# Optimization experiments

Measured on AMD Instinct MI355X. Metric: run time of the kernel, lower is better.

Reference implementation:

```python
import jax, jax.numpy as jnp
import numpy as np

T, B, H, L = 512, 64, 512, 2  # seq_len, batch, hidden(=input_size), num_layers


def setup_inputs() -> dict:
    key = jax.random.key(0)
    ks = jax.random.split(key, 5)
    std = 1.0 / np.sqrt(H)
    u = lambda k, s: jax.random.uniform(k, s, jnp.float32, -std, std)
    Wxh = u(ks[0], (L, 4 * H, H))   # [L, 4H, in] (in == H here)
    Whh = u(ks[1], (L, 4 * H, H))   # [L, 4H, H]
    bxh = u(ks[2], (L, 4 * H))
    bhh = u(ks[3], (L, 4 * H))
    # LSTMCell.reset_parameters sets the forget-gate bias slice [H:2H] to 1/H
    bxh = bxh.at[:, H:2 * H].set(1.0 / H)
    bhh = bhh.at[:, H:2 * H].set(1.0 / H)
    x = jax.random.normal(ks[4], (T, B, H), jnp.float32)  # [seq, batch, input]
    return {"x": x, "Wxh": Wxh, "Whh": Whh, "bxh": bxh, "bhh": bhh}


def _lstm_forward(x, Wxh, Whh, bxh, bhh):
    n_layers = Wxh.shape[0]
    bsz = x.shape[1]
    hid = Whh.shape[2]
    h0 = jnp.zeros((n_layers, bsz, hid), x.dtype)  # zero init (hc=None path)
    c0 = jnp.zeros((n_layers, bsz, hid), x.dtype)

    def step(carry, x_t):
        h, c = carry  # each [L, B, H]
        h_new, c_new = [], []
        inp = x_t  # [B, in]
        for l in range(n_layers):
            # gate order matches chunk(4): input, forget, cell, output
            gates = inp @ Wxh[l].T + bxh[l] + h[l] @ Whh[l].T + bhh[l]  # [B, 4H]
            i, f, g, o = jnp.split(gates, 4, axis=-1)
            c_l = jax.nn.sigmoid(f) * c[l] + jax.nn.sigmoid(i) * jnp.tanh(g)
            h_l = jax.nn.sigmoid(o) * jnp.tanh(c_l)
            h_new.append(h_l)
            c_new.append(c_l)
            inp = h_l  # feed to next layer
        return (jnp.stack(h_new), jnp.stack(c_new)), h_new[-1]

    (hT, cT), out = jax.lax.scan(step, (h0, c0), x)
    # out: [T, B, H] (top-layer hidden per step); hidden state tuple (h, c): [L, B, H]
    return out, (hT, cT)


def reference(x, Wxh, Whh, bxh, bhh):
    return _lstm_forward(x, Wxh, Whh, bxh, bhh)
```

## Files before the change

### kernel.cpp

```cpp
#include <hip/hip_runtime.h>


#define T_SEQ 512

typedef short s16x8 __attribute__((ext_vector_type(8)));
typedef int   i32x4 __attribute__((ext_vector_type(4)));
typedef float f32x4 __attribute__((ext_vector_type(4)));

__device__ __forceinline__ short f2bf(float f) {
    unsigned u = __builtin_bit_cast(unsigned, f);
    unsigned r = (u + 0x7fffu + ((u >> 16) & 1u)) >> 16;
    return (short)r;
}
__device__ __forceinline__ float sigf(float x) { return 1.0f / (1.0f + __expf(-x)); }
__device__ __forceinline__ float tanhff(float x) { return 2.0f * sigf(2.0f * x) - 1.0f; }

__global__ __launch_bounds__(256) void xcast_kernel(const float* __restrict__ x,
                                                    short* __restrict__ xb) {
    int i = (blockIdx.x * 256 + threadIdx.x) * 8;
    float4 a = *(const float4*)(x + i);
    float4 b = *(const float4*)(x + i + 4);
    s16x8 v;
    v[0]=f2bf(a.x); v[1]=f2bf(a.y); v[2]=f2bf(a.z); v[3]=f2bf(a.w);
    v[4]=f2bf(b.x); v[5]=f2bf(b.y); v[6]=f2bf(b.z); v[7]=f2bf(b.w);
    *(s16x8*)(xb + i) = v;
}

__global__ __launch_bounds__(256) void wpack_kernel(const float* __restrict__ Wxh,
                                                    const float* __restrict__ Whh,
                                                    short* __restrict__ wp) {
    int fg = blockIdx.x * 256 + threadIdx.x;
    int lane = fg & 63;
    int kk   = (fg >> 6)  & 7;
    int g    = (fg >> 9)  & 3;
    int w    = (fg >> 11) & 3;
    int bb   = (fg >> 13) & 31;
    int l    = (fg >> 18) & 1;
    int ksrc = w * 128 + (kk & 3) * 32 + (lane >> 4) * 8;
    int jp   = g * 512 + bb * 16 + (lane & 15);
    const float* src = (kk < 4) ? (Wxh + ((size_t)(l * 2048 + jp) * 512 + ksrc))
                                : (Whh + ((size_t)(l * 2048 + jp) * 512 + ksrc));
    float4 a = *(const float4*)src;
    float4 b = *(const float4*)(src + 4);
    s16x8 v;
    v[0]=f2bf(a.x); v[1]=f2bf(a.y); v[2]=f2bf(a.z); v[3]=f2bf(a.w);
    v[4]=f2bf(b.x); v[5]=f2bf(b.y); v[6]=f2bf(b.z); v[7]=f2bf(b.w);
    *(s16x8*)(wp + (size_t)fg * 8) = v;
}

__device__ __forceinline__ void load4_c(i32x4 af[4], const short* base) {
    asm volatile(
        "global_load_dwordx4 %0, %4, off sc0 sc1\n\t"
        "global_load_dwordx4 %1, %4, off offset:64 sc0 sc1\n\t"
        "global_load_dwordx4 %2, %4, off offset:128 sc0 sc1\n\t"
        "global_load_dwordx4 %3, %4, off offset:192 sc0 sc1\n\t"
        "s_waitcnt vmcnt(0)"
        : "=&v"(af[0]), "=&v"(af[1]), "=&v"(af[2]), "=&v"(af[3])
        : "v"(base)
        : "memory");
}

__device__ __forceinline__ void load8_c(i32x4 ar[4], i32x4 ai[4],
                                        const short* b0, const short* b1) {
    asm volatile(
        "global_load_dwordx4 %0, %8, off sc0 sc1\n\t"
        "global_load_dwordx4 %1, %8, off offset:64 sc0 sc1\n\t"
        "global_load_dwordx4 %2, %8, off offset:128 sc0 sc1\n\t"
        "global_load_dwordx4 %3, %8, off offset:192 sc0 sc1\n\t"
        "global_load_dwordx4 %4, %9, off sc0 sc1\n\t"
        "global_load_dwordx4 %5, %9, off offset:64 sc0 sc1\n\t"
        "global_load_dwordx4 %6, %9, off offset:128 sc0 sc1\n\t"
        "global_load_dwordx4 %7, %9, off offset:192 sc0 sc1\n\t"
        "s_waitcnt vmcnt(0)"
        : "=&v"(ar[0]), "=&v"(ar[1]), "=&v"(ar[2]), "=&v"(ar[3]),
          "=&v"(ai[0]), "=&v"(ai[1]), "=&v"(ai[2]), "=&v"(ai[3])
        : "v"(b0), "v"(b1)
        : "memory");
}

__device__ __forceinline__ void waitf2(const unsigned* fa, int ta,
                                       const unsigned* fb, int tb, int lane) {
    if (ta <= 0 && tb <= 0) return;
    const unsigned* pa = fa + (lane & 31);
    const unsigned* pb = fb + (lane & 31);
    int v0, v1;
    do {
        asm volatile("global_load_dword %0, %2, off sc0 sc1\n\t"
                     "global_load_dword %1, %3, off sc0 sc1\n\t"
                     "s_waitcnt vmcnt(0)"
                     : "=&v"(v0), "=&v"(v1)
                     : "v"(pa), "v"(pb) : "memory");
    } while (v0 < ta || v1 < tb);
}

__global__ __launch_bounds__(256, 1) void lstm_persist(
    const short* __restrict__ xb,
    const short* __restrict__ wp,
    short* __restrict__ h0r,
    short* __restrict__ h1r,
    const float* __restrict__ bxh,
    const float* __restrict__ bhh,
    float* __restrict__ out,
    unsigned* flags) {

    const int l    = blockIdx.x >> 7;
    const int g    = (blockIdx.x >> 5) & 3;
    const int bb   = blockIdx.x & 31;
    const int tid  = threadIdx.x;
    const int wv   = tid >> 6;
    const int lane = tid & 63;

    __shared__ float red[16 * 288];

    s16x8 breg[4][8];
    {
        const short* wb = wp + (size_t)((l * 32 + bb) * 4 + wv) * 16384 + lane * 8;
        #pragma unroll
        for (int g4 = 0; g4 < 4; ++g4)
            #pragma unroll
            for (int kk = 0; kk < 8; ++kk)
                breg[g4][kk] = *(const s16x8*)(wb + (g4 * 8 + kk) * 512);
    }

    const int em = tid >> 4;
    const int ec = tid & 15;
    const int ej = bb * 16 + ec;
    float bsum[4];
    #pragma unroll
    for (int g4 = 0; g4 < 4; ++g4)
        bsum[g4] = bxh[l * 2048 + g4 * 512 + ej] + bhh[l * 2048 + g4 * 512 + ej];

    float creg = 0.f;

    const int arow  = lane & 15;
    const int acol  = wv * 128 + (lane >> 4) * 8;
    const int aboff = (g * 16 + arow) * 512 + acol;

    const unsigned* fown = flags + (l * 4 + g) * 32;
    const unsigned* foth = flags + ((1 - l) * 4 + g) * 32;
    unsigned* myflag = flags + (l * 4 + g) * 32 + bb;

    for (int t = 0; t < T_SEQ; ++t) {
        f32x4 acc[4];
        #pragma unroll
        for (int g4 = 0; g4 < 4; ++g4)
            acc[g4] = (f32x4){0.f, 0.f, 0.f, 0.f};

        if (l == 0) {
            const short* ab = xb + (size_t)t * 32768 + aboff;
            s16x8 ax[4];
            #pragma unroll
            for (int kk = 0; kk < 4; ++kk)
                ax[kk] = *(const s16x8*)(ab + kk * 32);
            #pragma unroll
            for (int kk = 0; kk < 4; ++kk)
                #pragma unroll
                for (int g4 = 0; g4 < 4; ++g4)
                    acc[g4] = __builtin_amdgcn_mfma_f32_16x16x32_bf16(
                        ax[kk], breg[g4][kk], acc[g4], 0, 0, 0);
            waitf2(fown, t, foth, t - 7, lane);
            i32x4 af[4];
            load4_c(af, h0r + (size_t)(t & 7) * 32768 + aboff);
            #pragma unroll
            for (int kk = 0; kk < 4; ++kk)
                #pragma unroll
                for (int g4 = 0; g4 < 4; ++g4)
                    acc[g4] = __builtin_amdgcn_mfma_f32_16x16x32_bf16(
                        __builtin_bit_cast(s16x8, af[kk]),
                        breg[g4][4 + kk], acc[g4], 0, 0, 0);
        } else {
            waitf2(fown, t, foth, t + 1, lane);
            i32x4 af[4], ag[4];
            load8_c(af, ag, h1r + (size_t)(t & 7) * 32768 + aboff,
                            h0r + (size_t)((t + 1) & 7) * 32768 + aboff);
            #pragma unroll
            for (int kk = 0; kk < 4; ++kk)
                #pragma unroll
                for (int g4 = 0; g4 < 4; ++g4)
                    acc[g4] = __builtin_amdgcn_mfma_f32_16x16x32_bf16(
                        __builtin_bit_cast(s16x8, af[kk]),
                        breg[g4][4 + kk], acc[g4], 0, 0, 0);
            #pragma unroll
            for (int kk = 0; kk < 4; ++kk)
                #pragma unroll
                for (int g4 = 0; g4 < 4; ++g4)
                    acc[g4] = __builtin_amdgcn_mfma_f32_16x16x32_bf16(
                        __builtin_bit_cast(s16x8, ag[kk]),
                        breg[g4][kk], acc[g4], 0, 0, 0);
        }

        #pragma unroll
        for (int g4 = 0; g4 < 4; ++g4)
            #pragma unroll
            for (int q = 0; q < 4; ++q)
                red[(wv * 4 + g4) * 288
                    + ((lane >> 4) * 4 + q) * 18 + (lane & 15)] = acc[g4][q];
        __syncthreads();

        float cg[4];
        #pragma unroll
        for (int g4 = 0; g4 < 4; ++g4) {
            float s = bsum[g4];
            #pragma unroll
            for (int w = 0; w < 4; ++w)
                s += red[(w * 4 + g4) * 288 + em * 18 + ec];
            cg[g4] = s;
        }

        float cn = sigf(cg[1]) * creg + sigf(cg[0]) * tanhff(cg[2]);
        float hv = sigf(cg[3]) * tanhff(cn);
        creg = cn;

        {
            short* hring = (l == 0) ? h0r : h1r;
            short* hp = hring + (size_t)((t + 1) & 7) * 32768
                      + (g * 16 + em) * 512 + ej;
            int hb = (int)(unsigned short)f2bf(hv);
            asm volatile("global_store_short %0, %1, off sc0 sc1"
                         :: "v"(hp), "v"(hb) : "memory");
        }
        if (l == 1)
            out[(size_t)t * 32768 + (size_t)(g * 16 + em) * 512 + ej] = hv;
        if (t == T_SEQ - 1) {
            size_t base = (size_t)T_SEQ * 32768;
            out[base + (size_t)(l * 64 + g * 16 + em) * 512 + ej] = hv;
            out[base + 65536 + (size_t)(l * 64 + g * 16 + em) * 512 + ej] = creg;
        }

        asm volatile("s_waitcnt vmcnt(0)" ::: "memory");
        __syncthreads();
        if (tid == 0) {
            int fv = t + 1;
            asm volatile("global_store_dword %0, %1, off sc0 sc1"
                         :: "v"(myflag), "v"(fv) : "memory");
        }
    }
}

extern "C" void kernel_launch(void* const* d_in, const int* in_sizes, int n_in,
                              void* d_out, int out_size, void* d_ws, size_t ws_size,
                              hipStream_t stream) {
    const float* x   = (const float*)d_in[0];
    const float* Wxh = (const float*)d_in[1];
    const float* Whh = (const float*)d_in[2];
    const float* bxh = (const float*)d_in[3];
    const float* bhh = (const float*)d_in[4];
    float* out = (float*)d_out;

    char* ws = (char*)d_ws;
    short*    xb    = (short*)(ws);
    short*    wpk   = (short*)(ws + 33554432);
    short*    h0r   = (short*)(ws + 41943040);
    short*    h1r   = (short*)(ws + 42467328);
    unsigned* flags = (unsigned*)(ws + 42991616);

    hipMemsetAsync(ws + 41943040, 0, 1049600, stream);

    xcast_kernel<<<dim3(8192), dim3(256), 0, stream>>>(x, xb);
    wpack_kernel<<<dim3(2048), dim3(256), 0, stream>>>(Wxh, Whh, wpk);

    lstm_persist<<<dim3(256), dim3(256), 0, stream>>>(xb, wpk, h0r, h1r,
                                                      bxh, bhh, out, flags);
}
```

Before: 1.877 ms.

## Prefetch sync flags speculatively and split layer loops to overlap polling with loads

Splits the persistent LSTM loop into separate layer-0 and layer-1 paths. Each path issues its flag reads early, before the x-projection MFMAs in layer 0 and after the previous step's flag store in layer 1, so the common case needs no blocking poll. In layer 1 the layer-0 hidden-state load is issued as soon as its own flag is satisfied, overlapping it with the wait on the layer-1 dependency. Empty asm barriers pin the weight and bias registers. The aim is to shorten the per-step cross-block synchronization latency on the serial critical path, at the cost of more intricate vmcnt ordering that must stay correct.

```diff
diff --git a/kernel.cpp b/kernel.cpp
--- a/kernel.cpp
+++ b/kernel.cpp
@@ -48,7 +48,7 @@
     *(s16x8*)(wp + (size_t)fg * 8) = v;
 }
 
-__device__ __forceinline__ void load4_c(i32x4 af[4], const short* base) {
+__device__ __forceinline__ void load4_l3(i32x4 af[4], const short* base) {
     asm volatile(
         "global_load_dwordx4 %0, %4, off sc0 sc1\n\t"
         "global_load_dwordx4 %1, %4, off offset:64 sc0 sc1\n\t"
@@ -56,42 +56,92 @@
         "global_load_dwordx4 %3, %4, off offset:192 sc0 sc1\n\t"
         "s_waitcnt vmcnt(0)"
         : "=&v"(af[0]), "=&v"(af[1]), "=&v"(af[2]), "=&v"(af[3])
-        : "v"(base)
-        : "memory");
-}
-
-__device__ __forceinline__ void load8_c(i32x4 ar[4], i32x4 ai[4],
-                                        const short* b0, const short* b1) {
+        : "v"(base) : "memory");
+}
+__device__ __forceinline__ void load4_l3_issue(i32x4 af[4], const short* base) {
     asm volatile(
-        "global_load_dwordx4 %0, %8, off sc0 sc1\n\t"
-        "global_load_dwordx4 %1, %8, off offset:64 sc0 sc1\n\t"
-        "global_load_dwordx4 %2, %8, off offset:128 sc0 sc1\n\t"
-        "global_load_dwordx4 %3, %8, off offset:192 sc0 sc1\n\t"
-        "global_load_dwordx4 %4, %9, off sc0 sc1\n\t"
-        "global_load_dwordx4 %5, %9, off offset:64 sc0 sc1\n\t"
-        "global_load_dwordx4 %6, %9, off offset:128 sc0 sc1\n\t"
-        "global_load_dwordx4 %7, %9, off offset:192 sc0 sc1\n\t"
-        "s_waitcnt vmcnt(0)"
-        : "=&v"(ar[0]), "=&v"(ar[1]), "=&v"(ar[2]), "=&v"(ar[3]),
-          "=&v"(ai[0]), "=&v"(ai[1]), "=&v"(ai[2]), "=&v"(ai[3])
-        : "v"(b0), "v"(b1)
-        : "memory");
-}
-
-__device__ __forceinline__ void waitf2(const unsigned* fa, int ta,
-                                       const unsigned* fb, int tb, int lane) {
-    if (ta <= 0 && tb <= 0) return;
+        "global_load_dwordx4 %0, %4, off sc0 sc1\n\t"
+        "global_load_dwordx4 %1, %4, off offset:64 sc0 sc1\n\t"
+        "global_load_dwordx4 %2, %4, off offset:128 sc0 sc1\n\t"
+        "global_load_dwordx4 %3, %4, off offset:192 sc0 sc1"
+        : "=&v"(af[0]), "=&v"(af[1]), "=&v"(af[2]), "=&v"(af[3])
+        : "v"(base) : "memory");
+}
+__device__ __forceinline__ void tie4(i32x4 af[4]) {
+    asm volatile("s_waitcnt vmcnt(0)"
+                 : "+v"(af[0]), "+v"(af[1]), "+v"(af[2]), "+v"(af[3]) :: "memory");
+}
+
+__device__ __forceinline__ void flag_issue(int* v0, int* v1,
+                                           const unsigned* fa, const unsigned* fb,
+                                           int lane) {
     const unsigned* pa = fa + (lane & 31);
     const unsigned* pb = fb + (lane & 31);
-    int v0, v1;
+    asm volatile("global_load_dword %0, %2, off sc0 sc1\n\t"
+                 "global_load_dword %1, %3, off sc0 sc1"
+                 : "=&v"(*v0), "=&v"(*v1) : "v"(pa), "v"(pb) : "memory");
+}
+__device__ __forceinline__ void tie2_0(int* a, int* b) {
+    asm volatile("s_waitcnt vmcnt(0)" : "+v"(*a), "+v"(*b) :: "memory");
+}
+__device__ __forceinline__ void tie2_1(int* a, int* b) {
+    asm volatile("s_waitcnt vmcnt(1)" : "+v"(*a), "+v"(*b) :: "memory");
+}
+
+__device__ __forceinline__ void pollf(const unsigned* f, int thr, int lane) {
+    if (thr <= 0) return;
+    const unsigned* p = f + (lane & 31);
+    int v;
     do {
-        asm volatile("global_load_dword %0, %2, off sc0 sc1\n\t"
-                     "global_load_dword %1, %3, off sc0 sc1\n\t"
+        asm volatile("global_load_dword %0, %1, off sc0 sc1\n\t"
                      "s_waitcnt vmcnt(0)"
-                     : "=&v"(v0), "=&v"(v1)
-                     : "v"(pa), "v"(pb) : "memory");
-    } while (v0 < ta || v1 < tb);
-}
+                     : "=&v"(v) : "v"(p) : "memory");
+    } while (v < thr);
+}
+__device__ __forceinline__ void pollf2(const unsigned* fa, int ta,
+                                       const unsigned* fb, int tb, int lane) {
+    const unsigned* p = (lane < 32) ? (fa + lane) : (fb + (lane - 32));
+    int thr = (lane < 32) ? ta : tb;
+    int v;
+    do {
+        asm volatile("global_load_dword %0, %1, off sc0 sc1\n\t"
+                     "s_waitcnt vmcnt(0)"
+                     : "=&v"(v) : "v"(p) : "memory");
+    } while (v < thr);
+}
+
+__device__ __forceinline__ void sth_l3(short* p, int bits) {
+    asm volatile("global_store_short %0, %1, off sc0 sc1" :: "v"(p), "v"(bits) : "memory");
+}
+__device__ __forceinline__ void stf_l3(unsigned* p, int v) {
+    asm volatile("global_store_dword %0, %1, off sc0 sc1" :: "v"(p), "v"(v) : "memory");
+}
+
+#define DRAIN() asm volatile("s_waitcnt vmcnt(0)" ::: "memory")
+
+#define MFMA16(FR, WS)                                                        \
+    _Pragma("unroll") for (int kk = 0; kk < 4; ++kk)                          \
+    _Pragma("unroll") for (int g4 = 0; g4 < 4; ++g4)                          \
+        acc[g4] = __builtin_amdgcn_mfma_f32_16x16x32_bf16(                    \
+            __builtin_bit_cast(s16x8, FR[kk]), breg[g4][(WS) + kk],           \
+            acc[g4], 0, 0, 0);
+
+#define REDUCE_EPILOGUE()                                                     \
+    _Pragma("unroll") for (int g4 = 0; g4 < 4; ++g4)                          \
+        _Pragma("unroll") for (int q = 0; q < 4; ++q)                         \
+            red[(wv * 4 + g4) * 288                                           \
+                + ((lane >> 4) * 4 + q) * 18 + (lane & 15)] = acc[g4][q];     \
+    __syncthreads();                                                          \
+    float cg[4];                                                              \
+    _Pragma("unroll") for (int g4 = 0; g4 < 4; ++g4) {                        \
+        float s = bsum[g4];                                                   \
+        _Pragma("unroll") for (int w = 0; w < 4; ++w)                         \
+            s += red[(w * 4 + g4) * 288 + em * 18 + ec];                      \
+        cg[g4] = s;                                                           \
+    }                                                                         \
+    float cn = sigf(cg[1]) * creg + sigf(cg[0]) * tanhff(cg[2]);              \
+    hv = sigf(cg[3]) * tanhff(cn);                                            \
+    creg = cn;
 
 __global__ __launch_bounds__(256, 1) void lstm_persist(
     const short* __restrict__ xb,
@@ -121,6 +171,11 @@
             for (int kk = 0; kk < 8; ++kk)
                 breg[g4][kk] = *(const s16x8*)(wb + (g4 * 8 + kk) * 512);
     }
+    #pragma unroll
+    for (int g4 = 0; g4 < 4; ++g4)
+        asm volatile("" : "+v"(breg[g4][0]), "+v"(breg[g4][1]), "+v"(breg[g4][2]),
+                          "+v"(breg[g4][3]), "+v"(breg[g4][4]), "+v"(breg[g4][5]),
+                          "+v"(breg[g4][6]), "+v"(breg[g4][7]));
 
     const int em = tid >> 4;
     const int ec = tid & 15;
@@ -129,8 +184,9 @@
     #pragma unroll
     for (int g4 = 0; g4 < 4; ++g4)
         bsum[g4] = bxh[l * 2048 + g4 * 512 + ej] + bhh[l * 2048 + g4 * 512 + ej];
-
-    float creg = 0.f;
+    asm volatile("" : "+v"(bsum[0]), "+v"(bsum[1]), "+v"(bsum[2]), "+v"(bsum[3]));
+
+    float creg = 0.f, hv = 0.f;
 
     const int arow  = lane & 15;
     const int acol  = wv * 128 + (lane >> 4) * 8;
@@ -138,103 +194,72 @@
 
     const unsigned* fown = flags + (l * 4 + g) * 32;
     const unsigned* foth = flags + ((1 - l) * 4 + g) * 32;
-    unsigned* myflag = flags + (l * 4 + g) * 32 + bb;
-
-    for (int t = 0; t < T_SEQ; ++t) {
-        f32x4 acc[4];
-        #pragma unroll
-        for (int g4 = 0; g4 < 4; ++g4)
-            acc[g4] = (f32x4){0.f, 0.f, 0.f, 0.f};
-
-        if (l == 0) {
+    unsigned* myflag = (unsigned*)fown + bb;
+
+    if (l == 0) {
+        for (int t = 0; t < T_SEQ; ++t) {
+            int pv0 = 0, pv1 = 0;
+            flag_issue(&pv0, &pv1, fown, foth, lane);
+
+            f32x4 acc[4];
+            #pragma unroll
+            for (int g4 = 0; g4 < 4; ++g4) acc[g4] = (f32x4){0.f,0.f,0.f,0.f};
+
             const short* ab = xb + (size_t)t * 32768 + aboff;
             s16x8 ax[4];
             #pragma unroll
             for (int kk = 0; kk < 4; ++kk)
                 ax[kk] = *(const s16x8*)(ab + kk * 32);
-            #pragma unroll
-            for (int kk = 0; kk < 4; ++kk)
-                #pragma unroll
-                for (int g4 = 0; g4 < 4; ++g4)
-                    acc[g4] = __builtin_amdgcn_mfma_f32_16x16x32_bf16(
-                        ax[kk], breg[g4][kk], acc[g4], 0, 0, 0);
-            waitf2(fown, t, foth, t - 7, lane);
+            MFMA16(ax, 0)
+
+            tie2_0(&pv0, &pv1);
+            if (pv0 < t || pv1 < t - 7) pollf2(fown, t, foth, t - 7, lane);
+
             i32x4 af[4];
-            load4_c(af, h0r + (size_t)(t & 7) * 32768 + aboff);
-            #pragma unroll
-            for (int kk = 0; kk < 4; ++kk)
-                #pragma unroll
-                for (int g4 = 0; g4 < 4; ++g4)
-                    acc[g4] = __builtin_amdgcn_mfma_f32_16x16x32_bf16(
-                        __builtin_bit_cast(s16x8, af[kk]),
-                        breg[g4][4 + kk], acc[g4], 0, 0, 0);
-        } else {
-            waitf2(fown, t, foth, t + 1, lane);
-            i32x4 af[4], ag[4];
-            load8_c(af, ag, h1r + (size_t)(t & 7) * 32768 + aboff,
-                            h0r + (size_t)((t + 1) & 7) * 32768 + aboff);
-            #pragma unroll
-            for (int kk = 0; kk < 4; ++kk)
-                #pragma unroll
-                for (int g4 = 0; g4 < 4; ++g4)
-                    acc[g4] = __builtin_amdgcn_mfma_f32_16x16x32_bf16(
-                        __builtin_bit_cast(s16x8, af[kk]),
-                        breg[g4][4 + kk], acc[g4], 0, 0, 0);
-            #pragma unroll
-            for (int kk = 0; kk < 4; ++kk)
-                #pragma unroll
-                for (int g4 = 0; g4 < 4; ++g4)
-                    acc[g4] = __builtin_amdgcn_mfma_f32_16x16x32_bf16(
-                        __builtin_bit_cast(s16x8, ag[kk]),
-                        breg[g4][kk], acc[g4], 0, 0, 0);
+            load4_l3(af, h0r + (size_t)(t & 7) * 32768 + aboff);
+            MFMA16(af, 4)
+
+            REDUCE_EPILOGUE()
+
+            sth_l3(h0r + (size_t)((t + 1) & 7) * 32768 + (g * 16 + em) * 512 + ej,
+                   (int)(unsigned short)f2bf(hv));
+            DRAIN();
+            __syncthreads();
+            if (tid == 0) stf_l3(myflag, t + 1);
         }
-
-        #pragma unroll
-        for (int g4 = 0; g4 < 4; ++g4)
-            #pragma unroll
-            for (int q = 0; q < 4; ++q)
-                red[(wv * 4 + g4) * 288
-                    + ((lane >> 4) * 4 + q) * 18 + (lane & 15)] = acc[g4][q];
-        __syncthreads();
-
-        float cg[4];
-        #pragma unroll
-        for (int g4 = 0; g4 < 4; ++g4) {
-            float s = bsum[g4];
-            #pragma unroll
-            for (int w = 0; w < 4; ++w)
-                s += red[(w * 4 + g4) * 288 + em * 18 + ec];
-            cg[g4] = s;
-        }
-
-        float cn = sigf(cg[1]) * creg + sigf(cg[0]) * tanhff(cg[2]);
-        float hv = sigf(cg[3]) * tanhff(cn);
-        creg = cn;
-
-        {
-            short* hring = (l == 0) ? h0r : h1r;
-            short* hp = hring + (size_t)((t + 1) & 7) * 32768
-                      + (g * 16 + em) * 512 + ej;
-            int hb = (int)(unsigned short)f2bf(hv);
-            asm volatile("global_store_short %0, %1, off sc0 sc1"
-                         :: "v"(hp), "v"(hb) : "memory");
-        }
-        if (l == 1)
+    } else {
+        int pw0 = 0, pw1 = 0;
+        for (int t = 0; t < T_SEQ; ++t) {
+            tie2_1(&pw0, &pw1);
+            if (pw1 < t + 1) pollf(foth, t + 1, lane);
+            i32x4 ag[4];
+            load4_l3_issue(ag, h0r + (size_t)((t + 1) & 7) * 32768 + aboff);
+            if (pw0 < t) pollf(fown, t, lane);
+            i32x4 af[4];
+            load4_l3(af, h1r + (size_t)(t & 7) * 32768 + aboff);
+            tie4(ag);
+
+            f32x4 acc[4];
+            #pragma unroll
+            for (int g4 = 0; g4 < 4; ++g4) acc[g4] = (f32x4){0.f,0.f,0.f,0.f};
+            MFMA16(af, 4)
+            MFMA16(ag, 0)
+
+            REDUCE_EPILOGUE()
+
+            sth_l3(h1r + (size_t)((t + 1) & 7) * 32768 + (g * 16 + em) * 512 + ej,
+                   (int)(unsigned short)f2bf(hv));
+            DRAIN();
+            __syncthreads();
+            if (tid == 0) stf_l3(myflag, t + 1);
+            flag_issue(&pw0, &pw1, fown, foth, lane);
             out[(size_t)t * 32768 + (size_t)(g * 16 + em) * 512 + ej] = hv;
-        if (t == T_SEQ - 1) {
-            size_t base = (size_t)T_SEQ * 32768;
-            out[base + (size_t)(l * 64 + g * 16 + em) * 512 + ej] = hv;
-            out[base + 65536 + (size_t)(l * 64 + g * 16 + em) * 512 + ej] = creg;
-        }
-
-        asm volatile("s_waitcnt vmcnt(0)" ::: "memory");
-        __syncthreads();
-        if (tid == 0) {
-            int fv = t + 1;
-            asm volatile("global_store_dword %0, %1, off sc0 sc1"
-                         :: "v"(myflag), "v"(fv) : "memory");
         }
     }
+
+    size_t base = (size_t)T_SEQ * 32768;
+    out[base + (size_t)(l * 64 + g * 16 + em) * 512 + ej] = hv;
+    out[base + 65536 + (size_t)(l * 64 + g * 16 + em) * 512 + ej] = creg;
 }
 
 extern "C" void kernel_launch(void* const* d_in, const int* in_sizes, int n_in,
```

Result: slower. 2.793 ms (+48.9%).

## Split K across eight waves per block in persistent LSTM kernel

Applied to the files above, without the earlier changes.

Doubles the threads per block from 256 to 512 so each of eight waves covers 64 of the K dimension instead of 128. This halves the per-wave weight registers, the per-step global loads and the MFMA chain length. The weight packing layout and the shared-memory reduction change to match, and only the first 256 threads do the gate nonlinearity and the stores. The cost is a larger LDS reduction over eight partials and more waves taking part in each per-step barrier.

```diff
diff --git a/kernel.cpp b/kernel.cpp
--- a/kernel.cpp
+++ b/kernel.cpp
@@ -31,14 +31,14 @@
                                                     short* __restrict__ wp) {
     int fg = blockIdx.x * 256 + threadIdx.x;
     int lane = fg & 63;
-    int kk   = (fg >> 6)  & 7;
-    int g    = (fg >> 9)  & 3;
-    int w    = (fg >> 11) & 3;
+    int kk   = (fg >> 6)  & 3;
+    int g    = (fg >> 8)  & 3;
+    int w    = (fg >> 10) & 7;
     int bb   = (fg >> 13) & 31;
     int l    = (fg >> 18) & 1;
-    int ksrc = w * 128 + (kk & 3) * 32 + (lane >> 4) * 8;
+    int ksrc = w * 64 + (kk & 1) * 32 + (lane >> 4) * 8;
     int jp   = g * 512 + bb * 16 + (lane & 15);
-    const float* src = (kk < 4) ? (Wxh + ((size_t)(l * 2048 + jp) * 512 + ksrc))
+    const float* src = (kk < 2) ? (Wxh + ((size_t)(l * 2048 + jp) * 512 + ksrc))
                                 : (Whh + ((size_t)(l * 2048 + jp) * 512 + ksrc));
     float4 a = *(const float4*)src;
     float4 b = *(const float4*)(src + 4);
@@ -48,32 +48,23 @@
     *(s16x8*)(wp + (size_t)fg * 8) = v;
 }
 
-__device__ __forceinline__ void load4_c(i32x4 af[4], const short* base) {
+__device__ __forceinline__ void load2_l3(i32x4 af[2], const short* base) {
+    asm volatile(
+        "global_load_dwordx4 %0, %2, off sc0 sc1\n\t"
+        "global_load_dwordx4 %1, %2, off offset:64 sc0 sc1\n\t"
+        "s_waitcnt vmcnt(0)"
+        : "=&v"(af[0]), "=&v"(af[1])
+        : "v"(base) : "memory");
+}
+__device__ __forceinline__ void load4_c(i32x4 ar[2], i32x4 ai[2],
+                                        const short* b0, const short* b1) {
     asm volatile(
         "global_load_dwordx4 %0, %4, off sc0 sc1\n\t"
         "global_load_dwordx4 %1, %4, off offset:64 sc0 sc1\n\t"
-        "global_load_dwordx4 %2, %4, off offset:128 sc0 sc1\n\t"
-        "global_load_dwordx4 %3, %4, off offset:192 sc0 sc1\n\t"
+        "global_load_dwordx4 %2, %5, off sc0 sc1\n\t"
+        "global_load_dwordx4 %3, %5, off offset:64 sc0 sc1\n\t"
         "s_waitcnt vmcnt(0)"
-        : "=&v"(af[0]), "=&v"(af[1]), "=&v"(af[2]), "=&v"(af[3])
-        : "v"(base)
-        : "memory");
-}
-
-__device__ __forceinline__ void load8_c(i32x4 ar[4], i32x4 ai[4],
-                                        const short* b0, const short* b1) {
-    asm volatile(
-        "global_load_dwordx4 %0, %8, off sc0 sc1\n\t"
-        "global_load_dwordx4 %1, %8, off offset:64 sc0 sc1\n\t"
-        "global_load_dwordx4 %2, %8, off offset:128 sc0 sc1\n\t"
-        "global_load_dwordx4 %3, %8, off offset:192 sc0 sc1\n\t"
-        "global_load_dwordx4 %4, %9, off sc0 sc1\n\t"
-        "global_load_dwordx4 %5, %9, off offset:64 sc0 sc1\n\t"
-        "global_load_dwordx4 %6, %9, off offset:128 sc0 sc1\n\t"
-        "global_load_dwordx4 %7, %9, off offset:192 sc0 sc1\n\t"
-        "s_waitcnt vmcnt(0)"
-        : "=&v"(ar[0]), "=&v"(ar[1]), "=&v"(ar[2]), "=&v"(ar[3]),
-          "=&v"(ai[0]), "=&v"(ai[1]), "=&v"(ai[2]), "=&v"(ai[3])
+        : "=&v"(ar[0]), "=&v"(ar[1]), "=&v"(ai[0]), "=&v"(ai[1])
         : "v"(b0), "v"(b1)
         : "memory");
 }
@@ -93,7 +84,23 @@
     } while (v0 < ta || v1 < tb);
 }
 
-__global__ __launch_bounds__(256, 1) void lstm_persist(
+__device__ __forceinline__ void sth_l3(short* p, int bits) {
+    asm volatile("global_store_short %0, %1, off sc0 sc1" :: "v"(p), "v"(bits) : "memory");
+}
+__device__ __forceinline__ void stf_l3(unsigned* p, int v) {
+    asm volatile("global_store_dword %0, %1, off sc0 sc1" :: "v"(p), "v"(v) : "memory");
+}
+
+#define DRAIN() asm volatile("s_waitcnt vmcnt(0)" ::: "memory")
+
+#define MFMA8(FR, WS)                                                         \
+    _Pragma("unroll") for (int kk = 0; kk < 2; ++kk)                          \
+    _Pragma("unroll") for (int g4 = 0; g4 < 4; ++g4)                          \
+        acc[g4] = __builtin_amdgcn_mfma_f32_16x16x32_bf16(                    \
+            __builtin_bit_cast(s16x8, FR[kk]), breg[g4][(WS) + kk],           \
+            acc[g4], 0, 0, 0);
+
+__global__ __launch_bounds__(512, 1) void lstm_persist(
     const short* __restrict__ xb,
     const short* __restrict__ wp,
     short* __restrict__ h0r,
@@ -110,83 +117,64 @@
     const int wv   = tid >> 6;
     const int lane = tid & 63;
 
-    __shared__ float red[16 * 288];
-
-    s16x8 breg[4][8];
+    __shared__ float red[32 * 288];
+
+    s16x8 breg[4][4];
     {
-        const short* wb = wp + (size_t)((l * 32 + bb) * 4 + wv) * 16384 + lane * 8;
+        const short* wb = wp + (size_t)((l * 32 + bb) * 8 + wv) * 8192 + lane * 8;
         #pragma unroll
         for (int g4 = 0; g4 < 4; ++g4)
             #pragma unroll
-            for (int kk = 0; kk < 8; ++kk)
-                breg[g4][kk] = *(const s16x8*)(wb + (g4 * 8 + kk) * 512);
+            for (int kk = 0; kk < 4; ++kk)
+                breg[g4][kk] = *(const s16x8*)(wb + (g4 * 4 + kk) * 512);
     }
-
-    const int em = tid >> 4;
+    #pragma unroll
+    for (int g4 = 0; g4 < 4; ++g4)
+        asm volatile("" : "+v"(breg[g4][0]), "+v"(breg[g4][1]),
+                          "+v"(breg[g4][2]), "+v"(breg[g4][3]));
+
+    const int em = (tid >> 4) & 15;
     const int ec = tid & 15;
     const int ej = bb * 16 + ec;
     float bsum[4];
     #pragma unroll
     for (int g4 = 0; g4 < 4; ++g4)
         bsum[g4] = bxh[l * 2048 + g4 * 512 + ej] + bhh[l * 2048 + g4 * 512 + ej];
-
-    float creg = 0.f;
+    asm volatile("" : "+v"(bsum[0]), "+v"(bsum[1]), "+v"(bsum[2]), "+v"(bsum[3]));
+
+    float creg = 0.f, hv = 0.f;
 
     const int arow  = lane & 15;
-    const int acol  = wv * 128 + (lane >> 4) * 8;
+    const int acol  = wv * 64 + (lane >> 4) * 8;
     const int aboff = (g * 16 + arow) * 512 + acol;
 
     const unsigned* fown = flags + (l * 4 + g) * 32;
     const unsigned* foth = flags + ((1 - l) * 4 + g) * 32;
-    unsigned* myflag = flags + (l * 4 + g) * 32 + bb;
+    unsigned* myflag = (unsigned*)fown + bb;
 
     for (int t = 0; t < T_SEQ; ++t) {
         f32x4 acc[4];
         #pragma unroll
-        for (int g4 = 0; g4 < 4; ++g4)
-            acc[g4] = (f32x4){0.f, 0.f, 0.f, 0.f};
+        for (int g4 = 0; g4 < 4; ++g4) acc[g4] = (f32x4){0.f, 0.f, 0.f, 0.f};
 
         if (l == 0) {
             const short* ab = xb + (size_t)t * 32768 + aboff;
-            s16x8 ax[4];
-            #pragma unroll
-            for (int kk = 0; kk < 4; ++kk)
+            s16x8 ax[2];
+            #pragma unroll
+            for (int kk = 0; kk < 2; ++kk)
                 ax[kk] = *(const s16x8*)(ab + kk * 32);
-            #pragma unroll
-            for (int kk = 0; kk < 4; ++kk)
-                #pragma unroll
-                for (int g4 = 0; g4 < 4; ++g4)
-                    acc[g4] = __builtin_amdgcn_mfma_f32_16x16x32_bf16(
-                        ax[kk], breg[g4][kk], acc[g4], 0, 0, 0);
+            MFMA8(ax, 0)
             waitf2(fown, t, foth, t - 7, lane);
-            i32x4 af[4];
-            load4_c(af, h0r + (size_t)(t & 7) * 32768 + aboff);
-            #pragma unroll
-            for (int kk = 0; kk < 4; ++kk)
-                #pragma unroll
-                for (int g4 = 0; g4 < 4; ++g4)
-                    acc[g4] = __builtin_amdgcn_mfma_f32_16x16x32_bf16(
-                        __builtin_bit_cast(s16x8, af[kk]),
-                        breg[g4][4 + kk], acc[g4], 0, 0, 0);
+            i32x4 af[2];
+            load2_l3(af, h0r + (size_t)(t & 7) * 32768 + aboff);
+            MFMA8(af, 2)
         } else {
             waitf2(fown, t, foth, t + 1, lane);
-            i32x4 af[4], ag[4];
-            load8_c(af, ag, h1r + (size_t)(t & 7) * 32768 + aboff,
+            i32x4 af[2], ag[2];
+            load4_c(af, ag, h1r + (size_t)(t & 7) * 32768 + aboff,
                             h0r + (size_t)((t + 1) & 7) * 32768 + aboff);
-            #pragma unroll
-            for (int kk = 0; kk < 4; ++kk)
-                #pragma unroll
-                for (int g4 = 0; g4 < 4; ++g4)
-                    acc[g4] = __builtin_amdgcn_mfma_f32_16x16x32_bf16(
-                        __builtin_bit_cast(s16x8, af[kk]),
-                        breg[g4][4 + kk], acc[g4], 0, 0, 0);
-            #pragma unroll
-            for (int kk = 0; kk < 4; ++kk)
-                #pragma unroll
-                for (int g4 = 0; g4 < 4; ++g4)
-                    acc[g4] = __builtin_amdgcn_mfma_f32_16x16x32_bf16(
-                        __builtin_bit_cast(s16x8, ag[kk]),
-                        breg[g4][kk], acc[g4], 0, 0, 0);
+            MFMA8(af, 2)
+            MFMA8(ag, 0)
         }
 
         #pragma unroll
@@ -197,42 +185,38 @@
                     + ((lane >> 4) * 4 + q) * 18 + (lane & 15)] = acc[g4][q];
         __syncthreads();
 
-        float cg[4];
-        #pragma unroll
-        for (int g4 = 0; g4 < 4; ++g4) {
-            float s = bsum[g4];
-            #pragma unroll
-            for (int w = 0; w < 4; ++w)
-                s += red[(w * 4 + g4) * 288 + em * 18 + ec];
-            cg[g4] = s;
-        }
-
-        float cn = sigf(cg[1]) * creg + sigf(cg[0]) * tanhff(cg[2]);
-        float hv = sigf(cg[3]) * tanhff(cn);
-        creg = cn;
-
-        {
+        if (tid < 256) {
+            float cg[4];
+            #pragma unroll
+            for (int g4 = 0; g4 < 4; ++g4) {
+                float s = bsum[g4];
+                #pragma unroll
+                for (int w = 0; w < 8; ++w)
+                    s += red[(w * 4 + g4) * 288 + em * 18 + ec];
+                cg[g4] = s;
+            }
+            float cn = sigf(cg[1]) * creg + sigf(cg[0]) * tanhff(cg[2]);
+            hv = sigf(cg[3]) * tanhff(cn);
+            creg = cn;
+
             short* hring = (l == 0) ? h0r : h1r;
             short* hp = hring + (size_t)((t + 1) & 7) * 32768
                       + (g * 16 + em) * 512 + ej;
-            int hb = (int)(unsigned short)f2bf(hv);
-            asm volatile("global_store_short %0, %1, off sc0 sc1"
-                         :: "v"(hp), "v"(hb) : "memory");
+            sth_l3(hp, (int)(unsigned short)f2bf(hv));
+            if (l == 1)
+                out[(size_t)t * 32768 + (size_t)(g * 16 + em) * 512 + ej] = hv;
+            if (t == T_SEQ - 1) {
+                size_t base = (size_t)T_SEQ * 32768;
+                out[base + (size_t)(l * 64 + g * 16 + em) * 512 + ej] = hv;
+                out[base + 65536 + (size_t)(l * 64 + g * 16 + em) * 512 + ej] = creg;
+            }
         }
-        if (l == 1)
-            out[(size_t)t * 32768 + (size_t)(g * 16 + em) * 512 + ej] = hv;
-        if (t == T_SEQ - 1) {
-            size_t base = (size_t)T_SEQ * 32768;
-            out[base + (size_t)(l * 64 + g * 16 + em) * 512 + ej] = hv;
-            out[base + 65536 + (size_t)(l * 64 + g * 16 + em) * 512 + ej] = creg;
-        }
-
-        asm volatile("s_waitcnt vmcnt(0)" ::: "memory");
+
+        DRAIN();
         __syncthreads();
         if (tid == 0) {
             int fv = t + 1;
-            asm volatile("global_store_dword %0, %1, off sc0 sc1"
-                         :: "v"(myflag), "v"(fv) : "memory");
+            stf_l3(myflag, fv);
         }
     }
 }
@@ -259,6 +243,6 @@
     xcast_kernel<<<dim3(8192), dim3(256), 0, stream>>>(x, xb);
     wpack_kernel<<<dim3(2048), dim3(256), 0, stream>>>(Wxh, Whh, wpk);
 
-    lstm_persist<<<dim3(256), dim3(256), 0, stream>>>(xb, wpk, h0r, h1r,
+    lstm_persist<<<dim3(256), dim3(512), 0, stream>>>(xb, wpk, h0r, h1r,
                                                       bxh, bhh, out, flags);
 }
```

After: 3.219 ms. 71.5% more time.
